# Kernel tuning notes

Measured on AMD Instinct MI355X. Metric: run time of the kernel, lower is better.

The kernel has to match this reference:

```python
import jax, jax.numpy as jnp
import numpy as np

B, N, D, DIM = 64, 512, 128, 128
NEG_INF = -1e9


def setup_inputs() -> dict:
    key = jax.random.key(0)
    k1, k2, k3, k4 = jax.random.split(key, 4)
    atom_query = jax.random.normal(k1, (B, N, D), dtype=jnp.float32)
    # binary atom-presence mask, broadcastable over feature dim
    mask = jax.random.randint(k2, (B, N, 1), 0, 2).astype(jnp.float32)
    s = 1.0 / np.sqrt(D)
    Wq = jax.random.normal(k3, (D, DIM), dtype=jnp.float32) * s
    Wk = jax.random.normal(k4, (D, DIM), dtype=jnp.float32) * s
    bq = jnp.zeros((DIM,), dtype=jnp.float32)
    bk = jnp.zeros((DIM,), dtype=jnp.float32)
    return {"atom_query": atom_query, "mask": mask, "Wq": Wq, "bq": bq, "Wk": Wk, "bk": bk}


def reference(atom_query, mask, Wq, bq, Wk, bk):
    # projections
    q = atom_query @ Wq + bq              # [B, N, dim]
    k = atom_query @ Wk + bk              # [B, N, dim]
    mq = mask * q                          # masked query
    mk = mask * k                          # masked key

    # energy[b,i,j] = mk[b,i] . mq[b,j], with diagonal zeroed, then summed over j.
    # sum_j energy[b,i,j] = mk[b,i] . (sum_j mq[b,j]) - mk[b,i] . mq[b,i]
    # (identical math to materializing the [B,N,N] energy and reducing)
    q_sum = mq.sum(axis=1)                                   # [B, dim]
    agg = jnp.einsum('bnd,bd->bn', mk, q_sum) - (mk * mq).sum(-1)  # [B, N]
    agg = agg[:, :, None] * mask                             # [B, N, 1]

    # euclidean normalize over atom axis (tf.linalg.normalize, axis=1)
    nrm = jnp.sqrt(jnp.sum(agg * agg, axis=1, keepdims=True))
    agg = agg / nrm

    # masked softmax over atoms
    agg = agg + (1.0 - mask) * NEG_INF
    attn = jax.nn.softmax(agg, axis=1)                       # [B, N, 1]

    # v_proj=False, kq_proj=True -> values are the key projection
    context = jnp.sum(mask * attn * k, axis=1)               # [B, dim]
    return attn, context
```

## Files before the change

### kernel.cpp

```cpp
#include <hip/hip_runtime.h>
#include <math.h>

#define NB 64
#define NN 512
#define ND 128

typedef __attribute__((ext_vector_type(8))) short short8;
typedef __attribute__((ext_vector_type(4))) float f32x4;

#define KV_OFF    0
#define QK_OFF    (NB*NN*ND)
#define WT_OFF    (QK_OFF + NB*NN)
#define QSUM_OFF  (WT_OFF + 16384)

__device__ inline unsigned short f2bf(float x) {
    unsigned int u = __float_as_uint(x);
    return (unsigned short)((u + 0x7FFFu + ((u >> 16) & 1u)) >> 16);
}

__global__ __launch_bounds__(256) void conv_w(
    const float* __restrict__ Wq, const float* __restrict__ Wk,
    unsigned short* __restrict__ Wt)
{
    const int idx = blockIdx.x * 256 + threadIdx.x;
    const int m = idx >> 14, rem = idx & 16383;
    const int k = rem >> 7, c = rem & 127;
    const float v = m ? Wk[k*ND + c] : Wq[k*ND + c];
    Wt[(m*ND + c)*ND + k] = f2bf(v);
}

__global__ __launch_bounds__(256, 1) void proj_mfma(
    const float* __restrict__ aq, const float* __restrict__ mask,
    const unsigned short* __restrict__ Wt,
    const float* __restrict__ bq, const float* __restrict__ bk,
    float* __restrict__ kv, float* __restrict__ qk, float* __restrict__ qsum)
{
    __shared__ __align__(16) unsigned short a_lds[128][136];
    __shared__ float mask_lds[128];
    __shared__ float qk_part[4][128];

    const int b    = blockIdx.x >> 2;
    const int m0   = (blockIdx.x & 3) << 7;
    const int t    = threadIdx.x;
    const int w    = t >> 6, lane = t & 63;
    const int quad = lane >> 4, l16 = lane & 15;

    {
        const float4* src = (const float4*)(aq + ((size_t)b*NN + m0)*ND);
        #pragma unroll
        for (int i = 0; i < 16; i++) {
            const int idx = t + 256*i;
            const int row = idx >> 5, c4 = idx & 31;
            const float4 v = src[idx];
            ushort4 o;
            o.x = f2bf(v.x); o.y = f2bf(v.y); o.z = f2bf(v.z); o.w = f2bf(v.w);
            *(ushort4*)&a_lds[row][c4*4] = o;
        }
        if (t < 128) mask_lds[t] = mask[b*NN + m0 + t];
    }

    short8 bfr[4][4];
    #pragma unroll
    for (int nt = 0; nt < 4; nt++) {
        const int col = (nt < 2) ? (w*32 + nt*16 + l16)
                                 : (ND + w*32 + (nt-2)*16 + l16);
        #pragma unroll
        for (int kc = 0; kc < 4; kc++)
            bfr[nt][kc] = *(const short8*)(Wt + col*ND + kc*32 + quad*8);
    }

    __syncthreads();

    f32x4 acc[8][4];
    #pragma unroll
    for (int m = 0; m < 8; m++)
        #pragma unroll
        for (int nt = 0; nt < 4; nt++)
            acc[m][nt] = (f32x4){0.f, 0.f, 0.f, 0.f};

    #pragma unroll
    for (int m = 0; m < 8; m++) {
        short8 afr[4];
        #pragma unroll
        for (int kc = 0; kc < 4; kc++)
            afr[kc] = *(const short8*)&a_lds[m*16 + l16][kc*32 + quad*8];
        #pragma unroll
        for (int nt = 0; nt < 4; nt++)
            #pragma unroll
            for (int kc = 0; kc < 4; kc++)
                acc[m][nt] = __builtin_amdgcn_mfma_f32_16x16x32_bf16(
                    afr[kc], bfr[nt][kc], acc[m][nt], 0, 0, 0);
    }

    float bv[4];
    #pragma unroll
    for (int nt = 0; nt < 2; nt++) bv[nt] = bq[w*32 + nt*16 + l16];
    #pragma unroll
    for (int nt = 2; nt < 4; nt++) bv[nt] = bk[w*32 + (nt-2)*16 + l16];
    #pragma unroll
    for (int m = 0; m < 8; m++)
        #pragma unroll
        for (int nt = 0; nt < 4; nt++)
            #pragma unroll
            for (int r = 0; r < 4; r++)
                acc[m][nt][r] += bv[nt];

    #pragma unroll
    for (int m = 0; m < 8; m++)
        #pragma unroll
        for (int r = 0; r < 4; r++) {
            const size_t row = (size_t)b*NN + m0 + m*16 + quad*4 + r;
            kv[row*ND + w*32 + l16]      = acc[m][2][r];
            kv[row*ND + w*32 + 16 + l16] = acc[m][3][r];
        }

    #pragma unroll
    for (int m = 0; m < 8; m++) {
        float p[4];
        #pragma unroll
        for (int r = 0; r < 4; r++)
            p[r] = acc[m][0][r]*acc[m][2][r] + acc[m][1][r]*acc[m][3][r];
        #pragma unroll
        for (int off = 1; off <= 8; off <<= 1)
            #pragma unroll
            for (int r = 0; r < 4; r++)
                p[r] += __shfl_xor(p[r], off);
        if (l16 == 0)
            #pragma unroll
            for (int r = 0; r < 4; r++)
                qk_part[w][m*16 + quad*4 + r] = p[r];
    }

    {
        float s0 = 0.f, s1 = 0.f;
        #pragma unroll
        for (int m = 0; m < 8; m++)
            #pragma unroll
            for (int r = 0; r < 4; r++) {
                const float mk = mask_lds[m*16 + quad*4 + r];
                s0 += mk * acc[m][0][r];
                s1 += mk * acc[m][1][r];
            }
        s0 += __shfl_xor(s0, 16); s0 += __shfl_xor(s0, 32);
        s1 += __shfl_xor(s1, 16); s1 += __shfl_xor(s1, 32);
        if (quad == 0) {
            atomicAdd(&qsum[b*ND + w*32 + l16],      s0);
            atomicAdd(&qsum[b*ND + w*32 + 16 + l16], s1);
        }
    }

    __syncthreads();
    if (t < 128)
        qk[(size_t)b*NN + m0 + t] =
            qk_part[0][t] + qk_part[1][t] + qk_part[2][t] + qk_part[3][t];
}

__global__ __launch_bounds__(512) void fused_attn(
    const float* __restrict__ mask, const float* __restrict__ kv,
    const float* __restrict__ qk, const float* __restrict__ qsum,
    float* __restrict__ out_attn, float* __restrict__ out_ctx)
{
    __shared__ float qs[128];
    __shared__ float agg_s[512];
    __shared__ float red[16];
    __shared__ float bc2[2];
    __shared__ float zred[8];
    __shared__ float zbc;
    __shared__ float ctx_part[16][32];

    const int b  = blockIdx.x >> 2;
    const int cg = blockIdx.x & 3;
    const int t = threadIdx.x, w = t >> 6, lane = t & 63;

    if (t < 128) qs[t] = qsum[b*ND + t];
    __syncthreads();
    const float q0 = qs[2*lane], q1 = qs[2*lane + 1];

    for (int i0 = 0; i0 < 64; i0 += 4) {
        float p[4];
        #pragma unroll
        for (int r = 0; r < 4; r++) {
            const int n = w*64 + i0 + r;
            const float2 kvv = *(const float2*)(kv + ((size_t)b*NN + n)*ND + 2*lane);
            p[r] = kvv.x*q0 + kvv.y*q1;
        }
        #pragma unroll
        for (int off = 1; off <= 32; off <<= 1)
            #pragma unroll
            for (int r = 0; r < 4; r++) p[r] += __shfl_xor(p[r], off);
        if (lane == 0) {
            #pragma unroll
            for (int r = 0; r < 4; r++) {
                const int n = w*64 + i0 + r;
                agg_s[n] = mask[(size_t)b*NN + n] * (p[r] - qk[(size_t)b*NN + n]);
            }
        }
    }
    __syncthreads();

    const float v  = agg_s[t];
    const bool um  = mask[(size_t)b*NN + t] != 0.f;
    float sq = v * v;
    float mx = um ? v : -3.0e38f;
    #pragma unroll
    for (int off = 1; off <= 32; off <<= 1) {
        sq += __shfl_xor(sq, off);
        mx = fmaxf(mx, __shfl_xor(mx, off));
    }
    if (lane == 0) { red[w] = sq; red[8 + w] = mx; }
    __syncthreads();
    if (t == 0) {
        float s = 0.f, m = -3.0e38f;
        #pragma unroll
        for (int i = 0; i < 8; i++) { s += red[i]; m = fmaxf(m, red[8 + i]); }
        bc2[0] = sqrtf(s);
        bc2[1] = m;
    }
    __syncthreads();
    const float nrm = bc2[0];
    const float M   = bc2[1];

    const float e = um ? expf((v - M) / nrm) : 0.f;
    float z = e;
    #pragma unroll
    for (int off = 1; off <= 32; off <<= 1) z += __shfl_xor(z, off);
    if (lane == 0) zred[w] = z;
    agg_s[t] = e;
    __syncthreads();
    if (t == 0) {
        float s = 0.f;
        #pragma unroll
        for (int i = 0; i < 8; i++) s += zred[i];
        zbc = s;
    }
    __syncthreads();
    const float Z = zbc;
    if (cg == 0) out_attn[(size_t)b*NN + t] = e / Z;

    const int col = cg*32 + (t & 31);
    const int rg  = t >> 5;
    float a = 0.f;
    for (int n = rg; n < NN; n += 16)
        a += agg_s[n] * kv[((size_t)b*NN + n)*ND + col];
    ctx_part[rg][t & 31] = a;
    __syncthreads();
    if (t < 32) {
        float s = 0.f;
        #pragma unroll
        for (int i = 0; i < 16; i++) s += ctx_part[i][t];
        out_ctx[(size_t)b*ND + cg*32 + t] = s / Z;
    }
}

extern "C" void kernel_launch(void* const* d_in, const int* in_sizes, int n_in,
                              void* d_out, int out_size, void* d_ws, size_t ws_size,
                              hipStream_t stream)
{
    const float* aq   = (const float*)d_in[0];
    const float* mask = (const float*)d_in[1];
    const float* Wq   = (const float*)d_in[2];
    const float* bq   = (const float*)d_in[3];
    const float* Wk   = (const float*)d_in[4];
    const float* bk   = (const float*)d_in[5];

    float* ws = (float*)d_ws;
    float*          kv   = ws + KV_OFF;
    float*          qk   = ws + QK_OFF;
    unsigned short* Wt   = (unsigned short*)(ws + WT_OFF);
    float*          qsum = ws + QSUM_OFF;

    float* out_attn = (float*)d_out;
    float* out_ctx  = (float*)d_out + NB*NN;

    hipMemsetAsync(qsum, 0, NB*ND*sizeof(float), stream);
    conv_w<<<dim3(128), dim3(256), 0, stream>>>(Wq, Wk, Wt);
    proj_mfma<<<dim3(256), dim3(256), 0, stream>>>(aq, mask, Wt, bq, bk, kv, qk, qsum);
    fused_attn<<<dim3(256), dim3(512), 0, stream>>>(mask, kv, qk, qsum, out_attn, out_ctx);
}
```

Measured before the change: 109.8 us.

## Store key projection in bf16 and replace qsum atomics with partial sums

The key-projection intermediate is now written as bf16 instead of fp32, halving the bytes moved between the projection and attention kernels. The qsum atomicAdd and its memset are replaced by per-block partial slots that the attention kernel sums itself, and the mask is staged in shared memory. The first dot product also uses wider per-lane loads with half-wave reductions. The cost is lost precision in the keys used for both the scores and the context output.

```diff
diff --git a/kernel.cpp b/kernel.cpp
--- a/kernel.cpp
+++ b/kernel.cpp
@@ -8,14 +8,17 @@
 typedef __attribute__((ext_vector_type(8))) short short8;
 typedef __attribute__((ext_vector_type(4))) float f32x4;
 
-#define KV_OFF    0
-#define QK_OFF    (NB*NN*ND)
+#define KVB_OFF   0
+#define QK_OFF    (NB*NN*ND/2)
 #define WT_OFF    (QK_OFF + NB*NN)
-#define QSUM_OFF  (WT_OFF + 16384)
+#define QSUMP_OFF (WT_OFF + 16384)
 
 __device__ inline unsigned short f2bf(float x) {
     unsigned int u = __float_as_uint(x);
     return (unsigned short)((u + 0x7FFFu + ((u >> 16) & 1u)) >> 16);
+}
+__device__ inline float bf2f(unsigned short u) {
+    return __uint_as_float(((unsigned int)u) << 16);
 }
 
 __global__ __launch_bounds__(256) void conv_w(
@@ -33,7 +36,8 @@
     const float* __restrict__ aq, const float* __restrict__ mask,
     const unsigned short* __restrict__ Wt,
     const float* __restrict__ bq, const float* __restrict__ bk,
-    float* __restrict__ kv, float* __restrict__ qk, float* __restrict__ qsum)
+    unsigned short* __restrict__ kvb, float* __restrict__ qk,
+    float* __restrict__ qsum_part)
 {
     __shared__ __align__(16) unsigned short a_lds[128][136];
     __shared__ float mask_lds[128];
@@ -110,8 +114,8 @@
         #pragma unroll
         for (int r = 0; r < 4; r++) {
             const size_t row = (size_t)b*NN + m0 + m*16 + quad*4 + r;
-            kv[row*ND + w*32 + l16]      = acc[m][2][r];
-            kv[row*ND + w*32 + 16 + l16] = acc[m][3][r];
+            kvb[row*ND + w*32 + l16]      = f2bf(acc[m][2][r]);
+            kvb[row*ND + w*32 + 16 + l16] = f2bf(acc[m][3][r]);
         }
 
     #pragma unroll
@@ -144,8 +148,9 @@
         s0 += __shfl_xor(s0, 16); s0 += __shfl_xor(s0, 32);
         s1 += __shfl_xor(s1, 16); s1 += __shfl_xor(s1, 32);
         if (quad == 0) {
-            atomicAdd(&qsum[b*ND + w*32 + l16],      s0);
-            atomicAdd(&qsum[b*ND + w*32 + 16 + l16], s1);
+            const int slot = (b*4 + (m0 >> 7)) * ND;
+            qsum_part[slot + w*32 + l16]      = s0;
+            qsum_part[slot + w*32 + 16 + l16] = s1;
         }
     }
 
@@ -156,11 +161,12 @@
 }
 
 __global__ __launch_bounds__(512) void fused_attn(
-    const float* __restrict__ mask, const float* __restrict__ kv,
-    const float* __restrict__ qk, const float* __restrict__ qsum,
+    const float* __restrict__ mask, const unsigned short* __restrict__ kvb,
+    const float* __restrict__ qk, const float* __restrict__ qsum_part,
     float* __restrict__ out_attn, float* __restrict__ out_ctx)
 {
     __shared__ float qs[128];
+    __shared__ float mask_s[512];
     __shared__ float agg_s[512];
     __shared__ float red[16];
     __shared__ float bc2[2];
@@ -171,35 +177,42 @@
     const int b  = blockIdx.x >> 2;
     const int cg = blockIdx.x & 3;
     const int t = threadIdx.x, w = t >> 6, lane = t & 63;
-
-    if (t < 128) qs[t] = qsum[b*ND + t];
-    __syncthreads();
-    const float q0 = qs[2*lane], q1 = qs[2*lane + 1];
+    const size_t rowbase = (size_t)b * NN;
+
+    if (t < 128)
+        qs[t] = qsum_part[(b*4 + 0)*ND + t] + qsum_part[(b*4 + 1)*ND + t]
+              + qsum_part[(b*4 + 2)*ND + t] + qsum_part[(b*4 + 3)*ND + t];
+    mask_s[t] = mask[rowbase + t];
+    __syncthreads();
+
+    const int h = lane & 31, half = lane >> 5;
+    float qsf[4];
+    #pragma unroll
+    for (int j = 0; j < 4; j++) qsf[j] = qs[h*4 + j];
 
     for (int i0 = 0; i0 < 64; i0 += 4) {
-        float p[4];
-        #pragma unroll
-        for (int r = 0; r < 4; r++) {
-            const int n = w*64 + i0 + r;
-            const float2 kvv = *(const float2*)(kv + ((size_t)b*NN + n)*ND + 2*lane);
-            p[r] = kvv.x*q0 + kvv.y*q1;
-        }
-        #pragma unroll
-        for (int off = 1; off <= 32; off <<= 1)
-            #pragma unroll
-            for (int r = 0; r < 4; r++) p[r] += __shfl_xor(p[r], off);
-        if (lane == 0) {
-            #pragma unroll
-            for (int r = 0; r < 4; r++) {
-                const int n = w*64 + i0 + r;
-                agg_s[n] = mask[(size_t)b*NN + n] * (p[r] - qk[(size_t)b*NN + n]);
-            }
+        const int na = w*64 + i0 + half;
+        const int nb2 = na + 2;
+        const ushort4 ka = *(const ushort4*)(kvb + (rowbase + na)*ND + h*4);
+        const ushort4 kb = *(const ushort4*)(kvb + (rowbase + nb2)*ND + h*4);
+        float p0 = bf2f(ka.x)*qsf[0] + bf2f(ka.y)*qsf[1]
+                 + bf2f(ka.z)*qsf[2] + bf2f(ka.w)*qsf[3];
+        float p1 = bf2f(kb.x)*qsf[0] + bf2f(kb.y)*qsf[1]
+                 + bf2f(kb.z)*qsf[2] + bf2f(kb.w)*qsf[3];
+        #pragma unroll
+        for (int off = 1; off <= 16; off <<= 1) {
+            p0 += __shfl_xor(p0, off);
+            p1 += __shfl_xor(p1, off);
+        }
+        if (h == 0) {
+            agg_s[na]  = mask_s[na]  * (p0 - qk[rowbase + na]);
+            agg_s[nb2] = mask_s[nb2] * (p1 - qk[rowbase + nb2]);
         }
     }
     __syncthreads();
 
     const float v  = agg_s[t];
-    const bool um  = mask[(size_t)b*NN + t] != 0.f;
+    const bool um  = mask_s[t] != 0.f;
     float sq = v * v;
     float mx = um ? v : -3.0e38f;
     #pragma unroll
@@ -235,13 +248,13 @@
     }
     __syncthreads();
     const float Z = zbc;
-    if (cg == 0) out_attn[(size_t)b*NN + t] = e / Z;
+    if (cg == 0) out_attn[rowbase + t] = e / Z;
 
     const int col = cg*32 + (t & 31);
     const int rg  = t >> 5;
     float a = 0.f;
     for (int n = rg; n < NN; n += 16)
-        a += agg_s[n] * kv[((size_t)b*NN + n)*ND + col];
+        a += agg_s[n] * bf2f(kvb[(rowbase + n)*ND + col]);
     ctx_part[rg][t & 31] = a;
     __syncthreads();
     if (t < 32) {
@@ -264,16 +277,15 @@
     const float* bk   = (const float*)d_in[5];
 
     float* ws = (float*)d_ws;
-    float*          kv   = ws + KV_OFF;
+    unsigned short* kvb  = (unsigned short*)(ws + KVB_OFF);
     float*          qk   = ws + QK_OFF;
     unsigned short* Wt   = (unsigned short*)(ws + WT_OFF);
-    float*          qsum = ws + QSUM_OFF;
+    float*          qsum_part = ws + QSUMP_OFF;
 
     float* out_attn = (float*)d_out;
     float* out_ctx  = (float*)d_out + NB*NN;
 
-    hipMemsetAsync(qsum, 0, NB*ND*sizeof(float), stream);
     conv_w<<<dim3(128), dim3(256), 0, stream>>>(Wq, Wk, Wt);
-    proj_mfma<<<dim3(256), dim3(256), 0, stream>>>(aq, mask, Wt, bq, bk, kv, qk, qsum);
-    fused_attn<<<dim3(256), dim3(512), 0, stream>>>(mask, kv, qk, qsum, out_attn, out_ctx);
-}
+    proj_mfma<<<dim3(256), dim3(256), 0, stream>>>(aq, mask, Wt, bq, bk, kvb, qk, qsum_part);
+    fused_attn<<<dim3(256), dim3(512), 0, stream>>>(mask, kvb, qk, qsum_part, out_attn, out_ctx);
+}
```

Result: faster. 104.4 us (-5.0%).
